# Optimization experiments

Measured on AMD Instinct MI355X. Metric: run time of the kernel, lower is better.

## Reference

```python
import jax, jax.numpy as jnp
import numpy as np

N_NODES = 50000
DROPOUT_P = 0.5


def _spmm(edge_src, edge_dst, edge_weight, h):
    # out[d] = sum_{e: dst[e]==d} w[e] * h[src[e]]  -- sparse Laplacian aggregation
    msgs = edge_weight[:, None] * h[edge_src]          # [E, F]
    return jax.ops.segment_sum(msgs, edge_dst, num_segments=N_NODES)


def setup_inputs() -> dict:
    key = jax.random.key(0)
    ks = jax.random.split(key, 8)
    E = 1600000
    nfeat, nhid, nclass = 512, 256, 40
    return {
        "x": jax.random.normal(ks[0], (N_NODES, nfeat), dtype=jnp.float32),
        "edge_src": jax.random.randint(ks[1], (E,), 0, N_NODES, dtype=jnp.int32),
        "edge_dst": jax.random.randint(ks[2], (E,), 0, N_NODES, dtype=jnp.int32),
        "edge_weight": jax.random.normal(ks[3], (E,), dtype=jnp.float32) * 0.05,
        "W1": jax.random.normal(ks[4], (nfeat, nhid), dtype=jnp.float32) * 0.05,
        "b1": jax.random.normal(ks[5], (nhid,), dtype=jnp.float32) * 0.05,
        "W2": jax.random.normal(ks[6], (nhid, nclass), dtype=jnp.float32) * 0.05,
        "b2": jax.random.normal(ks[7], (nclass,), dtype=jnp.float32) * 0.05,
    }


def reference(x, edge_src, edge_dst, edge_weight, W1, b1, W2, b2):
    # layer 1: dense GEMM -> sparse aggregate -> bias -> ReLU -> dropout
    h = x @ W1
    h = _spmm(edge_src, edge_dst, edge_weight, h)
    h = jax.nn.relu(h + b1)
    # dropout with a fixed key (deterministic, matches train-mode scaling 1/(1-p))
    keep = jax.random.bernoulli(jax.random.key(42), 1.0 - DROPOUT_P, h.shape)
    h = jnp.where(keep, h / (1.0 - DROPOUT_P), 0.0)
    # layer 2: dense GEMM -> sparse aggregate -> bias
    o = h @ W2
    o = _spmm(edge_src, edge_dst, edge_weight, o)
    return o + b2
```

## Files before the change

### kernel.cpp

```cpp
#include <hip/hip_runtime.h>

typedef short bf16x8 __attribute__((ext_vector_type(8)));
typedef float f32x4 __attribute__((ext_vector_type(4)));

constexpr int N_NODES = 50000;
constexpr int F_IN    = 512;
constexpr int F_HID   = 256;
constexpr int F_OUT   = 40;
constexpr int SCAN_BLOCKS = (N_NODES + 255) / 256;

__device__ __forceinline__ float bf2f(unsigned short u) {
  return __uint_as_float(((unsigned)u) << 16);
}
__device__ __forceinline__ unsigned short f2bf(float f) {
  unsigned x = __float_as_uint(f);
  x += 0x7FFFu + ((x >> 16) & 1u);
  return (unsigned short)(x >> 16);
}

__device__ __forceinline__ bf16x8 cvt8(f32x4 a, f32x4 b) {
  bf16x8 o;
  o[0] = (short)f2bf(a[0]); o[1] = (short)f2bf(a[1]);
  o[2] = (short)f2bf(a[2]); o[3] = (short)f2bf(a[3]);
  o[4] = (short)f2bf(b[0]); o[5] = (short)f2bf(b[1]);
  o[6] = (short)f2bf(b[2]); o[7] = (short)f2bf(b[3]);
  return o;
}

__device__ __forceinline__ unsigned tf_rotl(unsigned x, int d) {
  return (x << d) | (x >> (32 - d));
}
__device__ __forceinline__ unsigned threefry_bits(unsigned i) {
  const unsigned k0 = 0u, k1 = 42u, k2 = 0x1BD11BDAu ^ 0u ^ 42u;
  unsigned x0 = 0u + k0, x1 = i + k1;
#define TF_R(r) { x0 += x1; x1 = tf_rotl(x1, (r)) ^ x0; }
  TF_R(13) TF_R(15) TF_R(26) TF_R(6)   x0 += k1; x1 += k2 + 1u;
  TF_R(17) TF_R(29) TF_R(16) TF_R(24)  x0 += k2; x1 += k0 + 2u;
  TF_R(13) TF_R(15) TF_R(26) TF_R(6)   x0 += k0; x1 += k1 + 3u;
  TF_R(17) TF_R(29) TF_R(16) TF_R(24)  x0 += k1; x1 += k2 + 4u;
  TF_R(13) TF_R(15) TF_R(26) TF_R(6)   x0 += k2; x1 += k0 + 5u;
#undef TF_R
  return x0 ^ x1;
}

__global__ void k_zero(int* __restrict__ p, int n) {
  int i = blockIdx.x * 256 + threadIdx.x;
  if (i < n) p[i] = 0;
}

__global__ void k_hist(const int* __restrict__ dst, int* __restrict__ deg, int E) {
  int e = blockIdx.x * 256 + threadIdx.x;
  if (e < E) atomicAdd(&deg[dst[e]], 1);
}

__global__ __launch_bounds__(256) void k_scan_part(const int* __restrict__ deg,
                                                   int* __restrict__ bsum) {
  __shared__ int red[256];
  int t = threadIdx.x;
  int i = blockIdx.x * 256 + t;
  red[t] = (i < N_NODES) ? deg[i] : 0;
  __syncthreads();
#pragma unroll
  for (int off = 128; off > 0; off >>= 1) {
    if (t < off) red[t] += red[t + off];
    __syncthreads();
  }
  if (t == 0) bsum[blockIdx.x] = red[0];
}

__global__ __launch_bounds__(256) void k_scan_base(int* __restrict__ bsum,
                                                   int* __restrict__ offs) {
  __shared__ int sh[256];
  int t = threadIdx.x;
  int v = (t < SCAN_BLOCKS) ? bsum[t] : 0;
  sh[t] = v;
  __syncthreads();
#pragma unroll
  for (int off = 1; off < 256; off <<= 1) {
    int x = (t >= off) ? sh[t - off] : 0;
    __syncthreads();
    sh[t] += x;
    __syncthreads();
  }
  if (t < SCAN_BLOCKS) bsum[t] = sh[t] - v;
  if (t == 255) offs[N_NODES] = sh[255];
}

__global__ __launch_bounds__(256) void k_scan_final(int* __restrict__ deg,
                                                    const int* __restrict__ bsum,
                                                    int* __restrict__ offs) {
  __shared__ int sh[256];
  int t = threadIdx.x;
  int i = blockIdx.x * 256 + t;
  int v = (i < N_NODES) ? deg[i] : 0;
  sh[t] = v;
  __syncthreads();
#pragma unroll
  for (int off = 1; off < 256; off <<= 1) {
    int x = (t >= off) ? sh[t - off] : 0;
    __syncthreads();
    sh[t] += x;
    __syncthreads();
  }
  if (i < N_NODES) {
    offs[i] = bsum[blockIdx.x] + sh[t] - v;
    deg[i] = 0;
  }
}

__global__ void k_scatter(const int* __restrict__ src, const int* __restrict__ dst,
                          const float* __restrict__ w,
                          const int* __restrict__ offs, int* __restrict__ cursor,
                          unsigned* __restrict__ ep, int E) {
  int e = blockIdx.x * 256 + threadIdx.x;
  if (e < E) {
    int d = dst[e];
    int pos = offs[d] + atomicAdd(&cursor[d], 1);
    if (pos >= 0 && pos < E)
      ep[pos] = ((unsigned)src[e] << 16) | (unsigned)f2bf(w[e]);
  }
}

__global__ void k_wt(const float* __restrict__ W1, unsigned short* __restrict__ wT) {
  int i = blockIdx.x * 256 + threadIdx.x;
  if (i < F_IN * F_HID) {
    int c = i >> 9, k = i & 511;
    wT[i] = f2bf(W1[(size_t)k * F_HID + c]);
  }
}

__global__ __launch_bounds__(256, 4) void k_gemm1(const float* __restrict__ X,
                                                  const unsigned short* __restrict__ wT,
                                                  unsigned short* __restrict__ out,
                                                  int ldh, int half) {
  int t = threadIdx.x;
  int wave = t >> 6, lane = t & 63, q = lane >> 4, r = lane & 15;
  int halfsel, tile;
  if (half < 0) {
    halfsel = (blockIdx.x >> 3) & 1;
    tile = ((blockIdx.x >> 4) << 3) + (blockIdx.x & 7);
  } else {
    halfsel = half; tile = blockIdx.x;
  }
  int r0 = tile * 64;
  int colbase = (ldh == 256) ? halfsel * 128 : 0;
  int arow = r0 + wave * 16 + r;
  if (arow > N_NODES - 1) arow = N_NODES - 1;
  const float* xrow = X + (size_t)arow * F_IN + q * 8;
  const unsigned short* bl = wT + (size_t)halfsel * 128 * F_IN + (size_t)r * F_IN + q * 8;
  f32x4 acc[8];
#pragma unroll
  for (int n = 0; n < 8; ++n) acc[n] = (f32x4){0.f, 0.f, 0.f, 0.f};

  bf16x8 BA[8], BB[8];
#pragma unroll
  for (int n = 0; n < 8; ++n)
    BA[n] = *(const bf16x8*)(bl + (size_t)n * 16 * F_IN);

#pragma unroll
  for (int k0 = 0; k0 < F_IN; k0 += 64) {
    f32x4 a0 = *(const f32x4*)(xrow + k0);
    f32x4 a1 = *(const f32x4*)(xrow + k0 + 4);
    f32x4 a2 = *(const f32x4*)(xrow + k0 + 32);
    f32x4 a3 = *(const f32x4*)(xrow + k0 + 36);
    bf16x8 A0 = cvt8(a0, a1);
    bf16x8 A1 = cvt8(a2, a3);
#pragma unroll
    for (int n = 0; n < 8; ++n)
      BB[n] = *(const bf16x8*)(bl + (size_t)n * 16 * F_IN + k0 + 32);
#pragma unroll
    for (int n = 0; n < 8; ++n)
      acc[n] = __builtin_amdgcn_mfma_f32_16x16x32_bf16(A0, BA[n], acc[n], 0, 0, 0);
    if (k0 + 64 < F_IN) {
#pragma unroll
      for (int n = 0; n < 8; ++n)
        BA[n] = *(const bf16x8*)(bl + (size_t)n * 16 * F_IN + k0 + 64);
    }
#pragma unroll
    for (int n = 0; n < 8; ++n)
      acc[n] = __builtin_amdgcn_mfma_f32_16x16x32_bf16(A1, BB[n], acc[n], 0, 0, 0);
  }
  int mrow = r0 + wave * 16 + q * 4;
#pragma unroll
  for (int n = 0; n < 8; ++n) {
#pragma unroll
    for (int tt = 0; tt < 4; ++tt) {
      int row = mrow + tt;
      if (row < N_NODES)
        out[(size_t)row * ldh + colbase + n * 16 + r] = f2bf(acc[n][tt]);
    }
  }
}

__global__ __launch_bounds__(256) void k_agg1f(const ushort4* __restrict__ h14,
                                               const int* __restrict__ offs,
                                               const unsigned* __restrict__ ep,
                                               const float* __restrict__ b1,
                                               const float* __restrict__ W2,
                                               float* __restrict__ o1) {
  __shared__ unsigned short w2h[F_HID * F_OUT];
  __shared__ float hrow[4][F_HID];
  int t = threadIdx.x;
  for (int i = t; i < F_HID * F_OUT; i += 256)
    w2h[i] = f2bf(W2[i]);
  int wave = t >> 6, lane = t & 63;
  int wid = blockIdx.x * 4 + wave;
  int s0 = offs[wid], s1 = offs[wid + 1];
  float a0 = 0.f, a1 = 0.f, a2 = 0.f, a3 = 0.f;
  int e = s0;
  for (; e + 4 <= s1; e += 4) {
    unsigned p0 = ep[e], p1 = ep[e + 1], p2 = ep[e + 2], p3 = ep[e + 3];
    ushort4 v0 = h14[(size_t)(p0 >> 16) * 64 + lane];
    ushort4 v1 = h14[(size_t)(p1 >> 16) * 64 + lane];
    ushort4 v2 = h14[(size_t)(p2 >> 16) * 64 + lane];
    ushort4 v3 = h14[(size_t)(p3 >> 16) * 64 + lane];
    float w0 = bf2f((unsigned short)p0), w1 = bf2f((unsigned short)p1);
    float w2 = bf2f((unsigned short)p2), w3 = bf2f((unsigned short)p3);
    a0 = fmaf(w0, bf2f(v0.x), a0); a1 = fmaf(w0, bf2f(v0.y), a1);
    a2 = fmaf(w0, bf2f(v0.z), a2); a3 = fmaf(w0, bf2f(v0.w), a3);
    a0 = fmaf(w1, bf2f(v1.x), a0); a1 = fmaf(w1, bf2f(v1.y), a1);
    a2 = fmaf(w1, bf2f(v1.z), a2); a3 = fmaf(w1, bf2f(v1.w), a3);
    a0 = fmaf(w2, bf2f(v2.x), a0); a1 = fmaf(w2, bf2f(v2.y), a1);
    a2 = fmaf(w2, bf2f(v2.z), a2); a3 = fmaf(w2, bf2f(v2.w), a3);
    a0 = fmaf(w3, bf2f(v3.x), a0); a1 = fmaf(w3, bf2f(v3.y), a1);
    a2 = fmaf(w3, bf2f(v3.z), a2); a3 = fmaf(w3, bf2f(v3.w), a3);
  }
  for (; e < s1; ++e) {
    unsigned pe = ep[e];
    float w = bf2f((unsigned short)pe);
    ushort4 v = h14[(size_t)(pe >> 16) * 64 + lane];
    a0 = fmaf(w, bf2f(v.x), a0);
    a1 = fmaf(w, bf2f(v.y), a1);
    a2 = fmaf(w, bf2f(v.z), a2);
    a3 = fmaf(w, bf2f(v.w), a3);
  }
  int c0 = lane * 4;
  unsigned base = (unsigned)wid * 256u + (unsigned)c0;
  float r0 = fmaxf(a0 + b1[c0 + 0], 0.f);
  float r1 = fmaxf(a1 + b1[c0 + 1], 0.f);
  float r2 = fmaxf(a2 + b1[c0 + 2], 0.f);
  float r3 = fmaxf(a3 + b1[c0 + 3], 0.f);
  hrow[wave][c0 + 0] = (threefry_bits(base + 0u) >> 31) ? 0.f : r0 * 2.f;
  hrow[wave][c0 + 1] = (threefry_bits(base + 1u) >> 31) ? 0.f : r1 * 2.f;
  hrow[wave][c0 + 2] = (threefry_bits(base + 2u) >> 31) ? 0.f : r2 * 2.f;
  hrow[wave][c0 + 3] = (threefry_bits(base + 3u) >> 31) ? 0.f : r3 * 2.f;
  __syncthreads();
  if (lane < F_OUT) {
    float acc = 0.f;
#pragma unroll 8
    for (int k = 0; k < F_HID; ++k)
      acc = fmaf(hrow[wave][k], bf2f(w2h[k * F_OUT + lane]), acc);
    o1[(size_t)wid * F_OUT + lane] = acc;
  }
}

__global__ __launch_bounds__(256) void k_agg1h(const ushort2* __restrict__ h1h2,
                                               const int* __restrict__ offs,
                                               const unsigned* __restrict__ ep,
                                               const float* __restrict__ b1,
                                               const float* __restrict__ W2,
                                               float* __restrict__ o1, int half) {
  __shared__ unsigned short w2h[128 * F_OUT];
  __shared__ float hrow[4][128];
  int t = threadIdx.x;
  for (int i = t; i < 128 * F_OUT; i += 256) {
    int k = i / F_OUT, j = i - k * F_OUT;
    w2h[i] = f2bf(W2[(size_t)(half * 128 + k) * F_OUT + j]);
  }
  int wave = t >> 6, lane = t & 63;
  int wid = blockIdx.x * 4 + wave;
  int s0 = offs[wid], s1 = offs[wid + 1];
  float a0 = 0.f, a1 = 0.f;
  int e = s0;
  for (; e + 4 <= s1; e += 4) {
    unsigned p0 = ep[e], p1 = ep[e + 1], p2 = ep[e + 2], p3 = ep[e + 3];
    ushort2 v0 = h1h2[(size_t)(p0 >> 16) * 64 + lane];
    ushort2 v1 = h1h2[(size_t)(p1 >> 16) * 64 + lane];
    ushort2 v2 = h1h2[(size_t)(p2 >> 16) * 64 + lane];
    ushort2 v3 = h1h2[(size_t)(p3 >> 16) * 64 + lane];
    float w0 = bf2f((unsigned short)p0), w1 = bf2f((unsigned short)p1);
    float w2 = bf2f((unsigned short)p2), w3 = bf2f((unsigned short)p3);
    a0 = fmaf(w0, bf2f(v0.x), a0); a1 = fmaf(w0, bf2f(v0.y), a1);
    a0 = fmaf(w1, bf2f(v1.x), a0); a1 = fmaf(w1, bf2f(v1.y), a1);
    a0 = fmaf(w2, bf2f(v2.x), a0); a1 = fmaf(w2, bf2f(v2.y), a1);
    a0 = fmaf(w3, bf2f(v3.x), a0); a1 = fmaf(w3, bf2f(v3.y), a1);
  }
  for (; e < s1; ++e) {
    unsigned pe = ep[e];
    float w = bf2f((unsigned short)pe);
    ushort2 v = h1h2[(size_t)(pe >> 16) * 64 + lane];
    a0 = fmaf(w, bf2f(v.x), a0);
    a1 = fmaf(w, bf2f(v.y), a1);
  }
  int c0 = lane * 2;
  int gc = half * 128 + c0;
  float r0 = fmaxf(a0 + b1[gc + 0], 0.f);
  float r1 = fmaxf(a1 + b1[gc + 1], 0.f);
  unsigned base = (unsigned)wid * 256u + (unsigned)gc;
  r0 = (threefry_bits(base + 0u) >> 31) ? 0.f : r0 * 2.f;
  r1 = (threefry_bits(base + 1u) >> 31) ? 0.f : r1 * 2.f;
  hrow[wave][c0 + 0] = r0;
  hrow[wave][c0 + 1] = r1;
  __syncthreads();
  if (lane < F_OUT) {
    float acc = 0.f;
#pragma unroll 8
    for (int k = 0; k < 128; ++k)
      acc = fmaf(hrow[wave][k], bf2f(w2h[k * F_OUT + lane]), acc);
    o1[(size_t)wid * F_OUT + lane] += acc;
  }
}

__global__ __launch_bounds__(256) void k_agg2(const float* __restrict__ o1,
                                              const int* __restrict__ offs,
                                              const unsigned* __restrict__ ep,
                                              const float* __restrict__ b2,
                                              float* __restrict__ out) {
  int wid  = (blockIdx.x << 2) + (threadIdx.x >> 6);
  int lane = threadIdx.x & 63;
  if (lane >= F_OUT) return;
  int s0 = offs[wid], s1 = offs[wid + 1];
  float acc = 0.f;
  int e = s0;
  for (; e + 4 <= s1; e += 4) {
    unsigned p0 = ep[e], p1 = ep[e + 1], p2 = ep[e + 2], p3 = ep[e + 3];
    float g0 = o1[(size_t)(p0 >> 16) * F_OUT + lane];
    float g1 = o1[(size_t)(p1 >> 16) * F_OUT + lane];
    float g2 = o1[(size_t)(p2 >> 16) * F_OUT + lane];
    float g3 = o1[(size_t)(p3 >> 16) * F_OUT + lane];
    acc = fmaf(bf2f((unsigned short)p0), g0, acc);
    acc = fmaf(bf2f((unsigned short)p1), g1, acc);
    acc = fmaf(bf2f((unsigned short)p2), g2, acc);
    acc = fmaf(bf2f((unsigned short)p3), g3, acc);
  }
  for (; e < s1; ++e) {
    unsigned pe = ep[e];
    acc = fmaf(bf2f((unsigned short)pe), o1[(size_t)(pe >> 16) * F_OUT + lane], acc);
  }
  out[(size_t)wid * F_OUT + lane] = acc + b2[lane];
}

extern "C" void kernel_launch(void* const* d_in, const int* in_sizes, int n_in,
                              void* d_out, int out_size, void* d_ws, size_t ws_size,
                              hipStream_t stream) {
  const float* x    = (const float*)d_in[0];
  const int*   esrc = (const int*)d_in[1];
  const int*   edst = (const int*)d_in[2];
  const float* ew   = (const float*)d_in[3];
  const float* W1   = (const float*)d_in[4];
  const float* b1   = (const float*)d_in[5];
  const float* W2   = (const float*)d_in[6];
  const float* b2   = (const float*)d_in[7];
  const int E = in_sizes[1];

  auto rup = [](size_t b) { return (b + 255) & ~(size_t)255; };
  const size_t sz_h1full = rup((size_t)N_NODES * 256 * 2);
  const size_t sz_h1half = rup((size_t)N_NODES * 128 * 2);
  const size_t sz_o1     = rup((size_t)N_NODES * F_OUT * 4);
  const size_t sz_ep     = rup((size_t)E * 4);
  const size_t sz_wT     = rup((size_t)F_IN * F_HID * 2);
  const size_t sz_offs   = rup((size_t)(N_NODES + 1) * 4);
  const size_t sz_deg    = rup((size_t)N_NODES * 4);
  const size_t sz_bsum   = rup((size_t)SCAN_BLOCKS * 4);
  const size_t tail      = sz_o1 + sz_ep + sz_wT + sz_offs + sz_deg + sz_bsum;
  const bool   fused     = ws_size >= sz_h1full + tail;

  char* p = (char*)d_ws;
  auto alloc = [&](size_t bytes) { char* r = p; p += bytes; return r; };
  unsigned short* h1   = (unsigned short*)alloc(fused ? sz_h1full : sz_h1half);
  float*          o1   = (float*)alloc(sz_o1);
  unsigned*       ep   = (unsigned*)alloc(sz_ep);
  unsigned short* wT   = (unsigned short*)alloc(sz_wT);
  int*            offs = (int*)alloc(sz_offs);
  int*            deg  = (int*)alloc(sz_deg);
  int*            bsum = (int*)alloc(sz_bsum);

  int eb = (E + 255) / 256;
  k_zero<<<(N_NODES + 255) / 256, 256, 0, stream>>>(deg, N_NODES);
  k_wt<<<(F_IN * F_HID + 255) / 256, 256, 0, stream>>>(W1, wT);
  k_hist<<<eb, 256, 0, stream>>>(edst, deg, E);
  k_scan_part<<<SCAN_BLOCKS, 256, 0, stream>>>(deg, bsum);
  k_scan_base<<<1, 256, 0, stream>>>(bsum, offs);
  k_scan_final<<<SCAN_BLOCKS, 256, 0, stream>>>(deg, bsum, offs);
  k_scatter<<<eb, 256, 0, stream>>>(esrc, edst, ew, offs, deg, ep, E);

  int gblocks = (N_NODES + 63) / 64;
  if (fused) {
    int gpad = (gblocks + 7) & ~7;
    k_gemm1<<<gpad * 2, 256, 0, stream>>>(x, wT, h1, 256, -1);
    k_agg1f<<<N_NODES / 4, 256, 0, stream>>>((const ushort4*)h1, offs, ep, b1, W2, o1);
  } else {
    k_zero<<<(N_NODES * F_OUT + 255) / 256, 256, 0, stream>>>((int*)o1, N_NODES * F_OUT);
    for (int half = 0; half < 2; ++half) {
      k_gemm1<<<gblocks, 256, 0, stream>>>(x, wT, h1, 128, half);
      k_agg1h<<<N_NODES / 4, 256, 0, stream>>>((const ushort2*)h1, offs, ep, b1, W2, o1, half);
    }
  }
  k_agg2<<<N_NODES / 4, 256, 0, stream>>>(o1, offs, ep, b2, (float*)d_out);
}
```

Before: 640.2 us.

## Sort CSR edges by source bucket within each destination for gather locality

New measurement: 643.1 us. Within noise of the previous version (+0.5%).

```diff
diff --git a/kernel.cpp b/kernel.cpp
--- a/kernel.cpp
+++ b/kernel.cpp
@@ -8,6 +8,10 @@
 constexpr int F_HID   = 256;
 constexpr int F_OUT   = 40;
 constexpr int SCAN_BLOCKS = (N_NODES + 255) / 256;
+
+constexpr int NB  = 16;
+constexpr int N2  = N_NODES * NB;
+constexpr int SC2_BLOCKS = (N2 + 4095) / 4096;
 
 __device__ __forceinline__ float bf2f(unsigned short u) {
   return __uint_as_float(((unsigned)u) << 16);
@@ -69,10 +73,11 @@
 }
 
 __global__ __launch_bounds__(256) void k_scan_base(int* __restrict__ bsum,
-                                                   int* __restrict__ offs) {
+                                                   int* __restrict__ offs,
+                                                   int nparts, int ntot) {
   __shared__ int sh[256];
   int t = threadIdx.x;
-  int v = (t < SCAN_BLOCKS) ? bsum[t] : 0;
+  int v = (t < nparts) ? bsum[t] : 0;
   sh[t] = v;
   __syncthreads();
 #pragma unroll
@@ -82,8 +87,8 @@
     sh[t] += x;
     __syncthreads();
   }
-  if (t < SCAN_BLOCKS) bsum[t] = sh[t] - v;
-  if (t == 255) offs[N_NODES] = sh[255];
+  if (t < nparts) bsum[t] = sh[t] - v;
+  if (t == 255) offs[ntot] = sh[255];
 }
 
 __global__ __launch_bounds__(256) void k_scan_final(int* __restrict__ deg,
@@ -121,6 +126,71 @@
   }
 }
 
+__global__ void k_hist2(const int* __restrict__ src, const int* __restrict__ dst,
+                        int* __restrict__ deg2, int E) {
+  int e = blockIdx.x * 256 + threadIdx.x;
+  if (e < E) atomicAdd(&deg2[dst[e] * NB + (src[e] >> 12)], 1);
+}
+
+__global__ __launch_bounds__(1024) void k_scan2_part(const int* __restrict__ deg2,
+                                                     int* __restrict__ bsum) {
+  __shared__ int red[1024];
+  int t = threadIdx.x;
+  int i0 = blockIdx.x * 4096 + t * 4;
+  int s = 0;
+#pragma unroll
+  for (int k = 0; k < 4; ++k) { int i = i0 + k; if (i < N2) s += deg2[i]; }
+  red[t] = s;
+  __syncthreads();
+#pragma unroll
+  for (int off = 512; off > 0; off >>= 1) {
+    if (t < off) red[t] += red[t + off];
+    __syncthreads();
+  }
+  if (t == 0) bsum[blockIdx.x] = red[0];
+}
+
+__global__ __launch_bounds__(1024) void k_scan2_final(int* __restrict__ deg2,
+                                                      const int* __restrict__ bsum,
+                                                      int* __restrict__ offs2) {
+  __shared__ int sh[1024];
+  int t = threadIdx.x;
+  int i0 = blockIdx.x * 4096 + t * 4;
+  int v0 = (i0 + 0 < N2) ? deg2[i0 + 0] : 0;
+  int v1 = (i0 + 1 < N2) ? deg2[i0 + 1] : 0;
+  int v2 = (i0 + 2 < N2) ? deg2[i0 + 2] : 0;
+  int v3 = (i0 + 3 < N2) ? deg2[i0 + 3] : 0;
+  int tot = v0 + v1 + v2 + v3;
+  sh[t] = tot;
+  __syncthreads();
+#pragma unroll
+  for (int off = 1; off < 1024; off <<= 1) {
+    int x = (t >= off) ? sh[t - off] : 0;
+    __syncthreads();
+    sh[t] += x;
+    __syncthreads();
+  }
+  int run = bsum[blockIdx.x] + sh[t] - tot;
+  if (i0 + 0 < N2) { offs2[i0 + 0] = run;               deg2[i0 + 0] = 0; }
+  if (i0 + 1 < N2) { offs2[i0 + 1] = run + v0;          deg2[i0 + 1] = 0; }
+  if (i0 + 2 < N2) { offs2[i0 + 2] = run + v0 + v1;     deg2[i0 + 2] = 0; }
+  if (i0 + 3 < N2) { offs2[i0 + 3] = run + v0 + v1 + v2; deg2[i0 + 3] = 0; }
+}
+
+__global__ void k_scatter2(const int* __restrict__ src, const int* __restrict__ dst,
+                           const float* __restrict__ w,
+                           const int* __restrict__ offs2, int* __restrict__ cur2,
+                           unsigned* __restrict__ ep, int E) {
+  int e = blockIdx.x * 256 + threadIdx.x;
+  if (e < E) {
+    int s = src[e];
+    int key = dst[e] * NB + (s >> 12);
+    int pos = offs2[key] + atomicAdd(&cur2[key], 1);
+    if (pos >= 0 && pos < E)
+      ep[pos] = ((unsigned)s << 16) | (unsigned)f2bf(w[e]);
+  }
+}
+
 __global__ void k_wt(const float* __restrict__ W1, unsigned short* __restrict__ wT) {
   int i = blockIdx.x * 256 + threadIdx.x;
   if (i < F_IN * F_HID) {
@@ -197,7 +267,7 @@
                                                const unsigned* __restrict__ ep,
                                                const float* __restrict__ b1,
                                                const float* __restrict__ W2,
-                                               float* __restrict__ o1) {
+                                               float* __restrict__ o1, int ostride) {
   __shared__ unsigned short w2h[F_HID * F_OUT];
   __shared__ float hrow[4][F_HID];
   int t = threadIdx.x;
@@ -205,7 +275,7 @@
     w2h[i] = f2bf(W2[i]);
   int wave = t >> 6, lane = t & 63;
   int wid = blockIdx.x * 4 + wave;
-  int s0 = offs[wid], s1 = offs[wid + 1];
+  int s0 = offs[wid * ostride], s1 = offs[wid * ostride + ostride];
   float a0 = 0.f, a1 = 0.f, a2 = 0.f, a3 = 0.f;
   int e = s0;
   for (; e + 4 <= s1; e += 4) {
@@ -315,11 +385,11 @@
                                               const int* __restrict__ offs,
                                               const unsigned* __restrict__ ep,
                                               const float* __restrict__ b2,
-                                              float* __restrict__ out) {
+                                              float* __restrict__ out, int ostride) {
   int wid  = (blockIdx.x << 2) + (threadIdx.x >> 6);
   int lane = threadIdx.x & 63;
   if (lane >= F_OUT) return;
-  int s0 = offs[wid], s1 = offs[wid + 1];
+  int s0 = offs[wid * ostride], s1 = offs[wid * ostride + ostride];
   float acc = 0.f;
   int e = s0;
   for (; e + 4 <= s1; e += 4) {
@@ -361,40 +431,58 @@
   const size_t sz_wT     = rup((size_t)F_IN * F_HID * 2);
   const size_t sz_offs   = rup((size_t)(N_NODES + 1) * 4);
   const size_t sz_deg    = rup((size_t)N_NODES * 4);
-  const size_t sz_bsum   = rup((size_t)SCAN_BLOCKS * 4);
-  const size_t tail      = sz_o1 + sz_ep + sz_wT + sz_offs + sz_deg + sz_bsum;
-  const bool   fused     = ws_size >= sz_h1full + tail;
+  const size_t sz_offs2  = rup((size_t)(N2 + 1) * 4);
+  const size_t sz_deg2   = rup((size_t)N2 * 4);
+  const size_t sz_bsum   = rup((size_t)256 * 4);
+  const size_t tail_p    = sz_o1 + sz_ep + sz_wT + sz_offs + sz_deg + sz_bsum;
+  const size_t tail_b    = sz_o1 + sz_ep + sz_wT + sz_offs2 + sz_deg2 + sz_bsum;
+  const bool bucketed = ws_size >= sz_h1full + tail_b;
+  const bool fusedpl  = ws_size >= sz_h1full + tail_p;
 
   char* p = (char*)d_ws;
   auto alloc = [&](size_t bytes) { char* r = p; p += bytes; return r; };
-  unsigned short* h1   = (unsigned short*)alloc(fused ? sz_h1full : sz_h1half);
-  float*          o1   = (float*)alloc(sz_o1);
-  unsigned*       ep   = (unsigned*)alloc(sz_ep);
-  unsigned short* wT   = (unsigned short*)alloc(sz_wT);
-  int*            offs = (int*)alloc(sz_offs);
-  int*            deg  = (int*)alloc(sz_deg);
-  int*            bsum = (int*)alloc(sz_bsum);
+  unsigned short* h1 = (unsigned short*)alloc((bucketed || fusedpl) ? sz_h1full : sz_h1half);
+  float*    o1   = (float*)alloc(sz_o1);
+  unsigned* ep   = (unsigned*)alloc(sz_ep);
+  unsigned short* wT = (unsigned short*)alloc(sz_wT);
+  int* offs = (int*)alloc(bucketed ? sz_offs2 : sz_offs);
+  int* deg  = (int*)alloc(bucketed ? sz_deg2 : sz_deg);
+  int* bsum = (int*)alloc(sz_bsum);
 
   int eb = (E + 255) / 256;
-  k_zero<<<(N_NODES + 255) / 256, 256, 0, stream>>>(deg, N_NODES);
+  int gblocks = (N_NODES + 63) / 64;
   k_wt<<<(F_IN * F_HID + 255) / 256, 256, 0, stream>>>(W1, wT);
-  k_hist<<<eb, 256, 0, stream>>>(edst, deg, E);
-  k_scan_part<<<SCAN_BLOCKS, 256, 0, stream>>>(deg, bsum);
-  k_scan_base<<<1, 256, 0, stream>>>(bsum, offs);
-  k_scan_final<<<SCAN_BLOCKS, 256, 0, stream>>>(deg, bsum, offs);
-  k_scatter<<<eb, 256, 0, stream>>>(esrc, edst, ew, offs, deg, ep, E);
-
-  int gblocks = (N_NODES + 63) / 64;
-  if (fused) {
+
+  if (bucketed) {
+    k_zero<<<(N2 + 255) / 256, 256, 0, stream>>>(deg, N2);
+    k_hist2<<<eb, 256, 0, stream>>>(esrc, edst, deg, E);
+    k_scan2_part<<<SC2_BLOCKS, 1024, 0, stream>>>(deg, bsum);
+    k_scan_base<<<1, 256, 0, stream>>>(bsum, offs, SC2_BLOCKS, N2);
+    k_scan2_final<<<SC2_BLOCKS, 1024, 0, stream>>>(deg, bsum, offs);
+    k_scatter2<<<eb, 256, 0, stream>>>(esrc, edst, ew, offs, deg, ep, E);
     int gpad = (gblocks + 7) & ~7;
     k_gemm1<<<gpad * 2, 256, 0, stream>>>(x, wT, h1, 256, -1);
-    k_agg1f<<<N_NODES / 4, 256, 0, stream>>>((const ushort4*)h1, offs, ep, b1, W2, o1);
+    k_agg1f<<<N_NODES / 4, 256, 0, stream>>>((const ushort4*)h1, offs, ep, b1, W2, o1, NB);
+    k_agg2<<<N_NODES / 4, 256, 0, stream>>>(o1, offs, ep, b2, (float*)d_out, NB);
   } else {
-    k_zero<<<(N_NODES * F_OUT + 255) / 256, 256, 0, stream>>>((int*)o1, N_NODES * F_OUT);
-    for (int half = 0; half < 2; ++half) {
-      k_gemm1<<<gblocks, 256, 0, stream>>>(x, wT, h1, 128, half);
-      k_agg1h<<<N_NODES / 4, 256, 0, stream>>>((const ushort2*)h1, offs, ep, b1, W2, o1, half);
+    k_zero<<<(N_NODES + 255) / 256, 256, 0, stream>>>(deg, N_NODES);
+    k_hist<<<eb, 256, 0, stream>>>(edst, deg, E);
+    k_scan_part<<<SCAN_BLOCKS, 256, 0, stream>>>(deg, bsum);
+    k_scan_base<<<1, 256, 0, stream>>>(bsum, offs, SCAN_BLOCKS, N_NODES);
+    k_scan_final<<<SCAN_BLOCKS, 256, 0, stream>>>(deg, bsum, offs);
+    k_scatter<<<eb, 256, 0, stream>>>(esrc, edst, ew, offs, deg, ep, E);
+    if (fusedpl) {
+      int gpad = (gblocks + 7) & ~7;
+      k_gemm1<<<gpad * 2, 256, 0, stream>>>(x, wT, h1, 256, -1);
+      k_agg1f<<<N_NODES / 4, 256, 0, stream>>>((const ushort4*)h1, offs, ep, b1, W2, o1, 1);
+      k_agg2<<<N_NODES / 4, 256, 0, stream>>>(o1, offs, ep, b2, (float*)d_out, 1);
+    } else {
+      k_zero<<<(N_NODES * F_OUT + 255) / 256, 256, 0, stream>>>((int*)o1, N_NODES * F_OUT);
+      for (int half = 0; half < 2; ++half) {
+        k_gemm1<<<gblocks, 256, 0, stream>>>(x, wT, h1, 128, half);
+        k_agg1h<<<N_NODES / 4, 256, 0, stream>>>((const ushort2*)h1, offs, ep, b1, W2, o1, half);
+      }
+      k_agg2<<<N_NODES / 4, 256, 0, stream>>>(o1, offs, ep, b2, (float*)d_out, 1);
     }
   }
-  k_agg2<<<N_NODES / 4, 256, 0, stream>>>(o1, offs, ep, b2, (float*)d_out);
-}
+}
```
